# Kernel tuning notes

Measured on AMD Instinct MI355X. Metric: run time of the kernel, lower is better.

Reference implementation:

```python
import jax, jax.numpy as jnp
import numpy as np
import math

DIM, HEADS = 512, 8
D_K = DIM // HEADS

def setup_inputs() -> dict:
    key = jax.random.key(0)
    ks = jax.random.split(key, 6)
    B, LK, LQ = 16, 2048, 256
    s = 1.0 / math.sqrt(DIM)
    return {
        "L": jax.random.normal(ks[0], (B, LK, DIM), jnp.float32),
        "G": jax.random.normal(ks[1], (B, LQ, DIM), jnp.float32),
        "Wq": jax.random.normal(ks[2], (DIM, DIM), jnp.float32) * s,
        "bq": jnp.zeros((DIM,), jnp.float32),
        "Wo": jax.random.normal(ks[3], (DIM, DIM), jnp.float32) * s,
        "bo": jnp.zeros((DIM,), jnp.float32),
    }

def reference(L, G, Wq, bq, Wo, bo):
    B = G.shape[0]
    # Q projection from global tokens; K,V are raw local features split into heads
    q = (G @ Wq + bq).reshape(B, -1, HEADS, D_K)          # [B, Lq, H, d]
    k = L.reshape(B, -1, HEADS, D_K)                      # [B, Lk, H, d]
    v = k
    # double scaling as in source: / sqrt(d_k) * dim**-0.5
    scale = (D_K ** -0.5) * (DIM ** -0.5)
    dots = jnp.einsum("bqhd,bkhd->bhqk", q, k) * scale    # [B, H, Lq, Lk]
    attn = jax.nn.softmax(dots, axis=-1)
    x = jnp.einsum("bhqk,bkhd->bqhd", attn, v)            # [B, Lq, H, d]
    x = x.reshape(B, -1, HEADS * D_K)
    return x @ Wo + bo
```

## Files before the change

### kernel.cpp

```cpp
#include <hip/hip_runtime.h>

#define KSTR 72

typedef __attribute__((ext_vector_type(8))) short short8;
typedef __attribute__((ext_vector_type(4))) float f32x4;

#define EXP2F(x) __builtin_amdgcn_exp2f(x)

__device__ __forceinline__ unsigned short f2bf(float f) {
    union { float f; unsigned u; } v; v.f = f;
    unsigned r = v.u + 0x7fff + ((v.u >> 16) & 1);
    return (unsigned short)(r >> 16);
}
__device__ __forceinline__ unsigned pk2(float a, float b) {
    return (unsigned)f2bf(a) | ((unsigned)f2bf(b) << 16);
}

__global__ __launch_bounds__(256) void conv_prep(const float* __restrict__ Lmat,
                                                 const float* __restrict__ Wq,
                                                 const float* __restrict__ Wo,
                                                 unsigned short* __restrict__ KF,
                                                 unsigned short* __restrict__ VF,
                                                 unsigned short* __restrict__ WqF,
                                                 unsigned short* __restrict__ WoF) {
    const int tid = threadIdx.x;
    if (blockIdx.x >= 4096) {
        const int idx = blockIdx.x - 4096;
        const float* W = (idx >> 7) ? Wo : Wq;
        unsigned short* WF = (idx >> 7) ? WoF : WqF;
        int g = (idx & 127) * 256 + tid;
        int lane = g & 63, ntg = (g >> 6) & 31, kt = g >> 11;
        int c = lane & 15, quad = lane >> 4;
        const float* wp = W + (size_t)(32 * kt + 8 * quad) * 512 + 16 * ntg + c;
        float v[8];
        #pragma unroll
        for (int j = 0; j < 8; j++) v[j] = wp[(size_t)j * 512];
        uint4 u;
        u.x = pk2(v[0], v[1]); u.y = pk2(v[2], v[3]);
        u.z = pk2(v[4], v[5]); u.w = pk2(v[6], v[7]);
        *(uint4*)(WF + (size_t)g * 8) = u;
        return;
    }
    __shared__ unsigned short KFs[4096];
    __shared__ unsigned short VFs[4096];
    const int blk = blockIdx.x;
    const int t = blk & 31, h = (blk >> 5) & 7, b = blk >> 8;
    const int key = tid & 63, wv = tid >> 6;

    const float* src = Lmat + ((size_t)(b * 2048 + 64 * t + key)) * 512 + 64 * h + 16 * wv;
    float4 a0 = *(const float4*)src;
    float4 a1 = *(const float4*)(src + 4);
    float4 a2 = *(const float4*)(src + 8);
    float4 a3 = *(const float4*)(src + 12);
    float vals[16] = {a0.x, a0.y, a0.z, a0.w, a1.x, a1.y, a1.z, a1.w,
                      a2.x, a2.y, a2.z, a2.w, a3.x, a3.y, a3.z, a3.w};
    #pragma unroll
    for (int i = 0; i < 16; i++) {
        int d = 16 * wv + i;
        unsigned short bv = f2bf(vals[i]);
        KFs[((((key >> 4) * 2 + (d >> 5)) * 64) + ((d >> 3) & 3) * 16 + (key & 15)) * 8 + (d & 7)] = bv;
        VFs[((((d >> 4) * 2 + (key >> 5)) * 64) + ((key >> 3) & 3) * 16 + (d & 15)) * 8 + (key & 7)] = bv;
    }
    __syncthreads();
    size_t gbase = (size_t)blk * 4096 + tid * 16;
    *(uint4*)(KF + gbase)     = *(const uint4*)&KFs[tid * 16];
    *(uint4*)(KF + gbase + 8) = *(const uint4*)&KFs[tid * 16 + 8];
    *(uint4*)(VF + gbase)     = *(const uint4*)&VFs[tid * 16];
    *(uint4*)(VF + gbase + 8) = *(const uint4*)&VFs[tid * 16 + 8];
}

template<bool A_BF16, bool OUT_BF16>
__global__ __launch_bounds__(256, 2) void gemm_direct(const void* __restrict__ Ap,
                                                      const unsigned short* __restrict__ WF,
                                                      const float* __restrict__ bias,
                                                      void* __restrict__ Cp,
                                                      float oscale) {
    const int tid = threadIdx.x;
    const int wv = tid >> 6, lane = tid & 63;
    const int c = lane & 15, quad = lane >> 4;
    const int m0 = blockIdx.x * 64, n0 = blockIdx.y * 64;
    const int row = m0 + 16 * wv + c;

    f32x4 acc[4];
    #pragma unroll
    for (int nt = 0; nt < 4; nt++) acc[nt] = (f32x4){0.f, 0.f, 0.f, 0.f};

    #pragma unroll
    for (int kk = 0; kk < 16; kk++) {
        short8 af;
        if (A_BF16) {
            af = *(const short8*)((const unsigned short*)Ap + (size_t)row * 512 + 32 * kk + 8 * quad);
        } else {
            const float* ap = (const float*)Ap + (size_t)row * 512 + 32 * kk + 8 * quad;
            float4 x0 = *(const float4*)ap;
            float4 x1 = *(const float4*)(ap + 4);
            af[0] = (short)f2bf(x0.x); af[1] = (short)f2bf(x0.y);
            af[2] = (short)f2bf(x0.z); af[3] = (short)f2bf(x0.w);
            af[4] = (short)f2bf(x1.x); af[5] = (short)f2bf(x1.y);
            af[6] = (short)f2bf(x1.z); af[7] = (short)f2bf(x1.w);
        }
        #pragma unroll
        for (int nt = 0; nt < 4; nt++) {
            short8 bf = *(const short8*)(WF +
                (((size_t)kk * 32 + (n0 >> 4) + nt) * 64 + lane) * 8);
            acc[nt] = __builtin_amdgcn_mfma_f32_16x16x32_bf16(af, bf, acc[nt], 0, 0, 0);
        }
    }

    #pragma unroll
    for (int nt = 0; nt < 4; nt++) {
        float bv = bias[n0 + 16 * nt + c];
        #pragma unroll
        for (int r = 0; r < 4; r++) {
            float v = (acc[nt][r] + bv) * oscale;
            size_t idx = (size_t)(m0 + 16 * wv + 4 * quad + r) * 512 + n0 + 16 * nt + c;
            if (OUT_BF16) ((unsigned short*)Cp)[idx] = f2bf(v);
            else          ((float*)Cp)[idx] = v;
        }
    }
}

__global__ __launch_bounds__(256, 2) void attn_frag(const float* __restrict__ G,
                                                    const unsigned short* __restrict__ WqF,
                                                    const float* __restrict__ bq,
                                                    const unsigned short* __restrict__ KF,
                                                    const unsigned short* __restrict__ VF,
                                                    unsigned short* __restrict__ X,
                                                    float SCe) {
    __shared__ __align__(16) char shm_raw[4 * 64 * 68 * 4];
    unsigned short (*Pw)[4][16 * KSTR] = (unsigned short (*)[4][16 * KSTR])shm_raw;
    unsigned short (*Qs)[72] = (unsigned short (*)[72])(shm_raw + 36864);
    float (*Mrg)[64][68] = (float (*)[64][68])shm_raw;

    const int raw = blockIdx.x;
    const int h  = raw & 7;
    const int qt = (raw >> 3) & 3;
    const int b  = raw >> 5;
    const int tid = threadIdx.x;
    const int wv = tid >> 6, lane = tid & 63;
    const int c = lane & 15, quad = lane >> 4;
    const int n0 = h * 64;

    {
        f32x4 qacc[4];
        #pragma unroll
        for (int nt = 0; nt < 4; nt++) qacc[nt] = (f32x4){0.f, 0.f, 0.f, 0.f};
        const float* gbase = G + ((size_t)(b * 256 + qt * 64 + 16 * wv + c)) * 512;
        #pragma unroll
        for (int kk = 0; kk < 16; kk++) {
            const float* ap = gbase + 32 * kk + 8 * quad;
            float4 x0 = *(const float4*)ap;
            float4 x1 = *(const float4*)(ap + 4);
            short8 af;
            af[0] = (short)f2bf(x0.x); af[1] = (short)f2bf(x0.y);
            af[2] = (short)f2bf(x0.z); af[3] = (short)f2bf(x0.w);
            af[4] = (short)f2bf(x1.x); af[5] = (short)f2bf(x1.y);
            af[6] = (short)f2bf(x1.z); af[7] = (short)f2bf(x1.w);
            #pragma unroll
            for (int nt = 0; nt < 4; nt++) {
                short8 bf = *(const short8*)(WqF +
                    (((size_t)kk * 32 + (n0 >> 4) + nt) * 64 + lane) * 8);
                qacc[nt] = __builtin_amdgcn_mfma_f32_16x16x32_bf16(af, bf, qacc[nt], 0, 0, 0);
            }
        }
        #pragma unroll
        for (int nt = 0; nt < 4; nt++) {
            float bv = bq[n0 + 16 * nt + c];
            #pragma unroll
            for (int r = 0; r < 4; r++)
                Qs[16 * wv + 4 * quad + r][16 * nt + c] =
                    f2bf((qacc[nt][r] + bv) * SCe);
        }
    }
    __syncthreads();

    short8 qa[4][2];
    #pragma unroll
    for (int g = 0; g < 4; g++) {
        qa[g][0] = *(const short8*)&Qs[16 * g + c][8 * quad];
        qa[g][1] = *(const short8*)&Qs[16 * g + c][32 + 8 * quad];
    }

    short8 ones;
    #pragma unroll
    for (int i = 0; i < 8; i++) ones[i] = (short)0x3F80;

    f32x4 oacc[4][4];
    #pragma unroll
    for (int g = 0; g < 4; g++)
        #pragma unroll
        for (int dt = 0; dt < 4; dt++) oacc[g][dt] = (f32x4){0.f, 0.f, 0.f, 0.f};
    f32x4 lacc[4];
    #pragma unroll
    for (int g = 0; g < 4; g++) lacc[g] = (f32x4){0.f, 0.f, 0.f, 0.f};

    const int swc = (c >> 3) & 1;
    const int swr = (quad >> 1) & 1;

    const unsigned short* kf = KF + ((size_t)((b * 8 + h) * 32)) * 4096 + lane * 8;
    const unsigned short* vf = VF + ((size_t)((b * 8 + h) * 32)) * 4096 + lane * 8;

    for (int i = 0; i < 8; i++) {
        const int T = wv + 4 * i;
        const unsigned short* kt = kf + (size_t)T * 4096;
        const unsigned short* vt = vf + (size_t)T * 4096;
        short8 kbuf[8], vbuf[8];
        #pragma unroll
        for (int f = 0; f < 8; f++) kbuf[f] = *(const short8*)(kt + f * 512);
        #pragma unroll
        for (int f = 0; f < 8; f++) vbuf[f] = *(const short8*)(vt + f * 512);

        #pragma unroll
        for (int g = 0; g < 4; g++) {
            f32x4 sacc[4];
            #pragma unroll
            for (int nt = 0; nt < 4; nt++) sacc[nt] = (f32x4){0.f, 0.f, 0.f, 0.f};
            __builtin_amdgcn_s_setprio(1);
            #pragma unroll
            for (int nt = 0; nt < 4; nt++)
                #pragma unroll
                for (int ks = 0; ks < 2; ks++)
                    sacc[nt] = __builtin_amdgcn_mfma_f32_16x16x32_bf16(
                        qa[g][ks], kbuf[nt * 2 + ks], sacc[nt], 0, 0, 0);
            __builtin_amdgcn_s_setprio(0);
            #pragma unroll
            for (int nt = 0; nt < 4; nt++)
                #pragma unroll
                for (int r = 0; r < 4; r++)
                    Pw[wv][g][(4 * quad + r) * KSTR + ((16 * nt + c) ^ (8 * swr))] =
                        f2bf(EXP2F(sacc[nt][r]));
        }
        #pragma unroll
        for (int g = 0; g < 4; g++) {
            short8 pa0 = *(const short8*)&Pw[wv][g][c * KSTR + 8 * (quad ^ swc)];
            short8 pa1 = *(const short8*)&Pw[wv][g][c * KSTR + 32 + 8 * (quad ^ swc)];
            __builtin_amdgcn_s_setprio(1);
            #pragma unroll
            for (int dt = 0; dt < 4; dt++) {
                oacc[g][dt] = __builtin_amdgcn_mfma_f32_16x16x32_bf16(pa0, vbuf[dt * 2], oacc[g][dt], 0, 0, 0);
                oacc[g][dt] = __builtin_amdgcn_mfma_f32_16x16x32_bf16(pa1, vbuf[dt * 2 + 1], oacc[g][dt], 0, 0, 0);
            }
            lacc[g] = __builtin_amdgcn_mfma_f32_16x16x32_bf16(pa0, ones, lacc[g], 0, 0, 0);
            lacc[g] = __builtin_amdgcn_mfma_f32_16x16x32_bf16(pa1, ones, lacc[g], 0, 0, 0);
            __builtin_amdgcn_s_setprio(0);
        }
    }

    __syncthreads();
    #pragma unroll
    for (int g = 0; g < 4; g++) {
        #pragma unroll
        for (int dt = 0; dt < 4; dt++)
            #pragma unroll
            for (int r = 0; r < 4; r++)
                Mrg[wv][g * 16 + 4 * quad + r][16 * dt + c] = oacc[g][dt][r];
        #pragma unroll
        for (int r = 0; r < 4; r++)
            Mrg[wv][g * 16 + 4 * quad + r][64] = lacc[g][r];
    }
    __syncthreads();
    {
        const int row = 16 * wv + c;
        float sum[16];
        #pragma unroll
        for (int j = 0; j < 16; j++) sum[j] = 0.f;
        float lsum = 0.f;
        #pragma unroll
        for (int ws = 0; ws < 4; ws++) {
            #pragma unroll
            for (int j = 0; j < 16; j++) sum[j] += Mrg[ws][row][16 * quad + j];
            lsum += Mrg[ws][row][64];
        }
        float inv = 1.f / lsum;
        unsigned short us[16];
        #pragma unroll
        for (int j = 0; j < 16; j++) us[j] = f2bf(sum[j] * inv);
        unsigned short* xp =
            X + ((size_t)(b * 256 + qt * 64 + row)) * 512 + h * 64 + 16 * quad;
        *(uint4*)(xp)     = *(uint4*)&us[0];
        *(uint4*)(xp + 8) = *(uint4*)&us[8];
    }
}

extern "C" void kernel_launch(void* const* d_in, const int* in_sizes, int n_in,
                              void* d_out, int out_size, void* d_ws, size_t ws_size,
                              hipStream_t stream) {
    const float* Lmat = (const float*)d_in[0];
    const float* G    = (const float*)d_in[1];
    const float* Wq   = (const float*)d_in[2];
    const float* bq   = (const float*)d_in[3];
    const float* Wo   = (const float*)d_in[4];
    const float* bo   = (const float*)d_in[5];
    float* out = (float*)d_out;

    const float SCe = 0.005524271728019903f * 1.4426950408889634f;

    unsigned short* Qws = (unsigned short*)d_ws;
    unsigned short* Xws = Qws + (size_t)2097152;
    unsigned short* WqF = Xws + (size_t)2097152;
    unsigned short* WoF = WqF + (size_t)262144;
    unsigned short* KF  = WoF + (size_t)262144;
    unsigned short* VF  = KF  + (size_t)16777216;

    conv_prep<<<4352, 256, 0, stream>>>(Lmat, Wq, Wo, KF, VF, WqF, WoF);
    attn_frag<<<512, 256, 0, stream>>>(G, WqF, bq, KF, VF, Xws, SCe);
    gemm_direct<true, false><<<dim3(64, 8), 256, 0, stream>>>(Xws, WoF, bo, out, 1.0f);
}
```

Measured before the change: 164.3 us.

## Stage K/V tiles through LDS with double-buffered async loads, split rows per wave

```diff
diff --git a/kernel.cpp b/kernel.cpp
--- a/kernel.cpp
+++ b/kernel.cpp
@@ -6,6 +6,8 @@
 typedef __attribute__((ext_vector_type(4))) float f32x4;
 
 #define EXP2F(x) __builtin_amdgcn_exp2f(x)
+#define WAITV(n) asm volatile("s_waitcnt vmcnt(" #n ")" ::: "memory")
+#define SCHEDB() __builtin_amdgcn_sched_barrier(0)
 
 __device__ __forceinline__ unsigned short f2bf(float f) {
     union { float f; unsigned u; } v; v.f = f;
@@ -127,10 +129,10 @@
                                                     const unsigned short* __restrict__ VF,
                                                     unsigned short* __restrict__ X,
                                                     float SCe) {
-    __shared__ __align__(16) char shm_raw[4 * 64 * 68 * 4];
-    unsigned short (*Pw)[4][16 * KSTR] = (unsigned short (*)[4][16 * KSTR])shm_raw;
-    unsigned short (*Qs)[72] = (unsigned short (*)[72])(shm_raw + 36864);
-    float (*Mrg)[64][68] = (float (*)[64][68])shm_raw;
+    __shared__ unsigned short Kr[2][4096];
+    __shared__ unsigned short Vr[2][4096];
+    __shared__ unsigned short Pw[4][16 * KSTR];
+    __shared__ unsigned short Qs[64][72];
 
     const int raw = blockIdx.x;
     const int h  = raw & 7;
@@ -174,112 +176,101 @@
     }
     __syncthreads();
 
-    short8 qa[4][2];
-    #pragma unroll
-    for (int g = 0; g < 4; g++) {
-        qa[g][0] = *(const short8*)&Qs[16 * g + c][8 * quad];
-        qa[g][1] = *(const short8*)&Qs[16 * g + c][32 + 8 * quad];
-    }
+    short8 qa[2];
+    qa[0] = *(const short8*)&Qs[16 * wv + c][8 * quad];
+    qa[1] = *(const short8*)&Qs[16 * wv + c][32 + 8 * quad];
 
     short8 ones;
     #pragma unroll
     for (int i = 0; i < 8; i++) ones[i] = (short)0x3F80;
 
-    f32x4 oacc[4][4];
-    #pragma unroll
-    for (int g = 0; g < 4; g++)
-        #pragma unroll
-        for (int dt = 0; dt < 4; dt++) oacc[g][dt] = (f32x4){0.f, 0.f, 0.f, 0.f};
-    f32x4 lacc[4];
-    #pragma unroll
-    for (int g = 0; g < 4; g++) lacc[g] = (f32x4){0.f, 0.f, 0.f, 0.f};
+    f32x4 oacc[4];
+    #pragma unroll
+    for (int dt = 0; dt < 4; dt++) oacc[dt] = (f32x4){0.f, 0.f, 0.f, 0.f};
+    f32x4 lacc = (f32x4){0.f, 0.f, 0.f, 0.f};
 
     const int swc = (c >> 3) & 1;
     const int swr = (quad >> 1) & 1;
 
-    const unsigned short* kf = KF + ((size_t)((b * 8 + h) * 32)) * 4096 + lane * 8;
-    const unsigned short* vf = VF + ((size_t)((b * 8 + h) * 32)) * 4096 + lane * 8;
-
-    for (int i = 0; i < 8; i++) {
-        const int T = wv + 4 * i;
-        const unsigned short* kt = kf + (size_t)T * 4096;
-        const unsigned short* vt = vf + (size_t)T * 4096;
-        short8 kbuf[8], vbuf[8];
-        #pragma unroll
-        for (int f = 0; f < 8; f++) kbuf[f] = *(const short8*)(kt + f * 512);
-        #pragma unroll
-        for (int f = 0; f < 8; f++) vbuf[f] = *(const short8*)(vt + f * 512);
-
-        #pragma unroll
-        for (int g = 0; g < 4; g++) {
-            f32x4 sacc[4];
-            #pragma unroll
-            for (int nt = 0; nt < 4; nt++) sacc[nt] = (f32x4){0.f, 0.f, 0.f, 0.f};
-            __builtin_amdgcn_s_setprio(1);
-            #pragma unroll
-            for (int nt = 0; nt < 4; nt++)
-                #pragma unroll
-                for (int ks = 0; ks < 2; ks++)
-                    sacc[nt] = __builtin_amdgcn_mfma_f32_16x16x32_bf16(
-                        qa[g][ks], kbuf[nt * 2 + ks], sacc[nt], 0, 0, 0);
-            __builtin_amdgcn_s_setprio(0);
-            #pragma unroll
-            for (int nt = 0; nt < 4; nt++)
-                #pragma unroll
-                for (int r = 0; r < 4; r++)
-                    Pw[wv][g][(4 * quad + r) * KSTR + ((16 * nt + c) ^ (8 * swr))] =
-                        f2bf(EXP2F(sacc[nt][r]));
-        }
-        #pragma unroll
-        for (int g = 0; g < 4; g++) {
-            short8 pa0 = *(const short8*)&Pw[wv][g][c * KSTR + 8 * (quad ^ swc)];
-            short8 pa1 = *(const short8*)&Pw[wv][g][c * KSTR + 32 + 8 * (quad ^ swc)];
-            __builtin_amdgcn_s_setprio(1);
-            #pragma unroll
-            for (int dt = 0; dt < 4; dt++) {
-                oacc[g][dt] = __builtin_amdgcn_mfma_f32_16x16x32_bf16(pa0, vbuf[dt * 2], oacc[g][dt], 0, 0, 0);
-                oacc[g][dt] = __builtin_amdgcn_mfma_f32_16x16x32_bf16(pa1, vbuf[dt * 2 + 1], oacc[g][dt], 0, 0, 0);
-            }
-            lacc[g] = __builtin_amdgcn_mfma_f32_16x16x32_bf16(pa0, ones, lacc[g], 0, 0, 0);
-            lacc[g] = __builtin_amdgcn_mfma_f32_16x16x32_bf16(pa1, ones, lacc[g], 0, 0, 0);
-            __builtin_amdgcn_s_setprio(0);
-        }
-    }
-
-    __syncthreads();
-    #pragma unroll
-    for (int g = 0; g < 4; g++) {
+    const unsigned short* kf0 = KF + ((size_t)((b * 8 + h) * 32)) * 4096;
+    const unsigned short* vf0 = VF + ((size_t)((b * 8 + h) * 32)) * 4096;
+
+#define STAGE(bs, tp) do { \
+        const unsigned short* ks_ = kf0 + (size_t)(tp) * 4096 + wv * 1024 + lane * 8; \
+        const unsigned short* vs_ = vf0 + (size_t)(tp) * 4096 + wv * 1024 + lane * 8; \
+        __builtin_amdgcn_global_load_lds((const unsigned int*)ks_, \
+            (unsigned int*)&Kr[bs][wv * 1024 + lane * 8], 16, 0, 0); \
+        __builtin_amdgcn_global_load_lds((const unsigned int*)(ks_ + 512), \
+            (unsigned int*)&Kr[bs][wv * 1024 + 512 + lane * 8], 16, 0, 0); \
+        __builtin_amdgcn_global_load_lds((const unsigned int*)vs_, \
+            (unsigned int*)&Vr[bs][wv * 1024 + lane * 8], 16, 0, 0); \
+        __builtin_amdgcn_global_load_lds((const unsigned int*)(vs_ + 512), \
+            (unsigned int*)&Vr[bs][wv * 1024 + 512 + lane * 8], 16, 0, 0); \
+    } while (0)
+
+    auto compute = [&](const unsigned short* kr, const unsigned short* vr) {
+        short8 kbuf[8];
+        #pragma unroll
+        for (int f = 0; f < 8; f++) kbuf[f] = *(const short8*)(kr + f * 512 + lane * 8);
+        f32x4 sacc[4];
+        #pragma unroll
+        for (int nt = 0; nt < 4; nt++) sacc[nt] = (f32x4){0.f, 0.f, 0.f, 0.f};
+        __builtin_amdgcn_s_setprio(1);
+        #pragma unroll
+        for (int nt = 0; nt < 4; nt++)
+            #pragma unroll
+            for (int ks = 0; ks < 2; ks++)
+                sacc[nt] = __builtin_amdgcn_mfma_f32_16x16x32_bf16(
+                    qa[ks], kbuf[nt * 2 + ks], sacc[nt], 0, 0, 0);
+        __builtin_amdgcn_s_setprio(0);
+        #pragma unroll
+        for (int nt = 0; nt < 4; nt++)
+            #pragma unroll
+            for (int r = 0; r < 4; r++)
+                Pw[wv][(4 * quad + r) * KSTR + ((16 * nt + c) ^ (8 * swr))] =
+                    f2bf(EXP2F(sacc[nt][r]));
+        short8 pa0 = *(const short8*)&Pw[wv][c * KSTR + 8 * (quad ^ swc)];
+        short8 pa1 = *(const short8*)&Pw[wv][c * KSTR + 32 + 8 * (quad ^ swc)];
+        short8 vbuf[8];
+        #pragma unroll
+        for (int f = 0; f < 8; f++) vbuf[f] = *(const short8*)(vr + f * 512 + lane * 8);
+        __builtin_amdgcn_s_setprio(1);
+        #pragma unroll
+        for (int dt = 0; dt < 4; dt++) {
+            oacc[dt] = __builtin_amdgcn_mfma_f32_16x16x32_bf16(pa0, vbuf[dt * 2], oacc[dt], 0, 0, 0);
+            oacc[dt] = __builtin_amdgcn_mfma_f32_16x16x32_bf16(pa1, vbuf[dt * 2 + 1], oacc[dt], 0, 0, 0);
+        }
+        lacc = __builtin_amdgcn_mfma_f32_16x16x32_bf16(pa0, ones, lacc, 0, 0, 0);
+        lacc = __builtin_amdgcn_mfma_f32_16x16x32_bf16(pa1, ones, lacc, 0, 0, 0);
+        __builtin_amdgcn_s_setprio(0);
+    };
+
+    STAGE(0, 0);
+    STAGE(1, 1);
+    for (int i = 0; i < 16; i++) {
+        WAITV(4); SCHEDB();
+        __syncthreads();
+        compute(&Kr[0][0], &Vr[0][0]);
+        __syncthreads();
+        if (i < 15) { STAGE(0, 2 * i + 2); WAITV(4); }
+        else        { WAITV(0); }
+        SCHEDB();
+        __syncthreads();
+        compute(&Kr[1][0], &Vr[1][0]);
+        __syncthreads();
+        if (i < 15) STAGE(1, 2 * i + 3);
+    }
+
+    #pragma unroll
+    for (int r = 0; r < 4; r++) {
+        float inv = 1.f / lacc[r];
+        size_t row = (size_t)(b * 256 + qt * 64 + 16 * wv + 4 * quad + r);
+        unsigned short* xp = X + row * 512 + h * 64;
         #pragma unroll
         for (int dt = 0; dt < 4; dt++)
-            #pragma unroll
-            for (int r = 0; r < 4; r++)
-                Mrg[wv][g * 16 + 4 * quad + r][16 * dt + c] = oacc[g][dt][r];
-        #pragma unroll
-        for (int r = 0; r < 4; r++)
-            Mrg[wv][g * 16 + 4 * quad + r][64] = lacc[g][r];
-    }
-    __syncthreads();
-    {
-        const int row = 16 * wv + c;
-        float sum[16];
-        #pragma unroll
-        for (int j = 0; j < 16; j++) sum[j] = 0.f;
-        float lsum = 0.f;
-        #pragma unroll
-        for (int ws = 0; ws < 4; ws++) {
-            #pragma unroll
-            for (int j = 0; j < 16; j++) sum[j] += Mrg[ws][row][16 * quad + j];
-            lsum += Mrg[ws][row][64];
-        }
-        float inv = 1.f / lsum;
-        unsigned short us[16];
-        #pragma unroll
-        for (int j = 0; j < 16; j++) us[j] = f2bf(sum[j] * inv);
-        unsigned short* xp =
-            X + ((size_t)(b * 256 + qt * 64 + row)) * 512 + h * 64 + 16 * quad;
-        *(uint4*)(xp)     = *(uint4*)&us[0];
-        *(uint4*)(xp + 8) = *(uint4*)&us[8];
-    }
+            xp[16 * dt + c] = f2bf(oacc[dt][r] * inv);
+    }
+#undef STAGE
 }
 
 extern "C" void kernel_launch(void* const* d_in, const int* in_sizes, int n_in,
```

Result: slower. 173.6 us (+5.7%).

## Prefetch K tiles into a double-buffered LDS ring with direct global-to-LDS loads

Applied to the files above, without the earlier changes.

```diff
diff --git a/kernel.cpp b/kernel.cpp
--- a/kernel.cpp
+++ b/kernel.cpp
@@ -6,6 +6,8 @@
 typedef __attribute__((ext_vector_type(4))) float f32x4;
 
 #define EXP2F(x) __builtin_amdgcn_exp2f(x)
+#define WAITV(n) asm volatile("s_waitcnt vmcnt(" #n ")" ::: "memory")
+#define SCHEDB() __builtin_amdgcn_sched_barrier(0)
 
 __device__ __forceinline__ unsigned short f2bf(float f) {
     union { float f; unsigned u; } v; v.f = f;
@@ -127,10 +129,11 @@
                                                     const unsigned short* __restrict__ VF,
                                                     unsigned short* __restrict__ X,
                                                     float SCe) {
-    __shared__ __align__(16) char shm_raw[4 * 64 * 68 * 4];
-    unsigned short (*Pw)[4][16 * KSTR] = (unsigned short (*)[4][16 * KSTR])shm_raw;
-    unsigned short (*Qs)[72] = (unsigned short (*)[72])(shm_raw + 36864);
-    float (*Mrg)[64][68] = (float (*)[64][68])shm_raw;
+    __shared__ __align__(16) char shm[65536 + 9216];
+    unsigned short (*Kring)[2][4096] = (unsigned short (*)[2][4096])shm;
+    unsigned short (*Pw)[16 * KSTR] = (unsigned short (*)[16 * KSTR])(shm + 65536);
+    unsigned short (*Qs)[72] = (unsigned short (*)[72])(shm + 65536);
+    float (*Mrg)[64][68] = (float (*)[64][68])shm;
 
     const int raw = blockIdx.x;
     const int h  = raw & 7;
@@ -140,6 +143,21 @@
     const int wv = tid >> 6, lane = tid & 63;
     const int c = lane & 15, quad = lane >> 4;
     const int n0 = h * 64;
+
+    const unsigned short* kf0 = KF + ((size_t)((b * 8 + h) * 32)) * 4096;
+    const unsigned short* vf0 = VF + ((size_t)((b * 8 + h) * 32)) * 4096;
+
+#define STAGEK(slot, tp) do { \
+        const unsigned short* ks_ = kf0 + (size_t)(tp) * 4096 + lane * 8; \
+        unsigned short* ld_ = &Kring[wv][slot][lane * 8]; \
+        _Pragma("unroll") \
+        for (int ch_ = 0; ch_ < 8; ch_++) \
+            __builtin_amdgcn_global_load_lds((const unsigned int*)(ks_ + ch_ * 512), \
+                (unsigned int*)(ld_ + ch_ * 512), 16, 0, 0); \
+    } while (0)
+
+    STAGEK(0, wv);
+    STAGEK(1, wv + 4);
 
     {
         f32x4 qacc[4];
@@ -180,6 +198,7 @@
         qa[g][0] = *(const short8*)&Qs[16 * g + c][8 * quad];
         qa[g][1] = *(const short8*)&Qs[16 * g + c][32 + 8 * quad];
     }
+    __syncthreads();
 
     short8 ones;
     #pragma unroll
@@ -197,16 +216,17 @@
     const int swc = (c >> 3) & 1;
     const int swr = (quad >> 1) & 1;
 
-    const unsigned short* kf = KF + ((size_t)((b * 8 + h) * 32)) * 4096 + lane * 8;
-    const unsigned short* vf = VF + ((size_t)((b * 8 + h) * 32)) * 4096 + lane * 8;
-
     for (int i = 0; i < 8; i++) {
         const int T = wv + 4 * i;
-        const unsigned short* kt = kf + (size_t)T * 4096;
-        const unsigned short* vt = vf + (size_t)T * 4096;
-        short8 kbuf[8], vbuf[8];
-        #pragma unroll
-        for (int f = 0; f < 8; f++) kbuf[f] = *(const short8*)(kt + f * 512);
+        const int s = i & 1;
+        WAITV(8); SCHEDB();
+
+        short8 kbuf[8];
+        #pragma unroll
+        for (int f = 0; f < 8; f++)
+            kbuf[f] = *(const short8*)&Kring[wv][s][f * 512 + lane * 8];
+        const unsigned short* vt = vf0 + (size_t)T * 4096 + lane * 8;
+        short8 vbuf[8];
         #pragma unroll
         for (int f = 0; f < 8; f++) vbuf[f] = *(const short8*)(vt + f * 512);
 
@@ -227,13 +247,10 @@
             for (int nt = 0; nt < 4; nt++)
                 #pragma unroll
                 for (int r = 0; r < 4; r++)
-                    Pw[wv][g][(4 * quad + r) * KSTR + ((16 * nt + c) ^ (8 * swr))] =
+                    Pw[wv][(4 * quad + r) * KSTR + ((16 * nt + c) ^ (8 * swr))] =
                         f2bf(EXP2F(sacc[nt][r]));
-        }
-        #pragma unroll
-        for (int g = 0; g < 4; g++) {
-            short8 pa0 = *(const short8*)&Pw[wv][g][c * KSTR + 8 * (quad ^ swc)];
-            short8 pa1 = *(const short8*)&Pw[wv][g][c * KSTR + 32 + 8 * (quad ^ swc)];
+            short8 pa0 = *(const short8*)&Pw[wv][c * KSTR + 8 * (quad ^ swc)];
+            short8 pa1 = *(const short8*)&Pw[wv][c * KSTR + 32 + 8 * (quad ^ swc)];
             __builtin_amdgcn_s_setprio(1);
             #pragma unroll
             for (int dt = 0; dt < 4; dt++) {
@@ -244,6 +261,8 @@
             lacc[g] = __builtin_amdgcn_mfma_f32_16x16x32_bf16(pa1, ones, lacc[g], 0, 0, 0);
             __builtin_amdgcn_s_setprio(0);
         }
+
+        if (i < 6) STAGEK(s, T + 8);
     }
 
     __syncthreads();
@@ -280,6 +299,7 @@
         *(uint4*)(xp)     = *(uint4*)&us[0];
         *(uint4*)(xp + 8) = *(uint4*)&us[8];
     }
+#undef STAGEK
 }
 
 extern "C" void kernel_launch(void* const* d_in, const int* in_sizes, int n_in,
```

New measurement: 167.1 us. About the same (+1.7%).

## Use eight waves per attention block and shrink P scratch to one tile per wave

Applied to the files above, without the earlier changes.

```diff
diff --git a/kernel.cpp b/kernel.cpp
--- a/kernel.cpp
+++ b/kernel.cpp
@@ -120,17 +120,17 @@
     }
 }
 
-__global__ __launch_bounds__(256, 2) void attn_frag(const float* __restrict__ G,
+__global__ __launch_bounds__(512, 4) void attn_frag(const float* __restrict__ G,
                                                     const unsigned short* __restrict__ WqF,
                                                     const float* __restrict__ bq,
                                                     const unsigned short* __restrict__ KF,
                                                     const unsigned short* __restrict__ VF,
                                                     unsigned short* __restrict__ X,
                                                     float SCe) {
-    __shared__ __align__(16) char shm_raw[4 * 64 * 68 * 4];
-    unsigned short (*Pw)[4][16 * KSTR] = (unsigned short (*)[4][16 * KSTR])shm_raw;
-    unsigned short (*Qs)[72] = (unsigned short (*)[72])(shm_raw + 36864);
-    float (*Mrg)[64][68] = (float (*)[64][68])shm_raw;
+    __shared__ __align__(16) char shm[4 * 64 * 68 * 4];
+    unsigned short (*Pw)[16 * KSTR] = (unsigned short (*)[16 * KSTR])shm;
+    unsigned short (*Qs)[72] = (unsigned short (*)[72])(shm + 18432);
+    float (*Mrg)[64][68] = (float (*)[64][68])shm;
 
     const int raw = blockIdx.x;
     const int h  = raw & 7;
@@ -141,7 +141,7 @@
     const int c = lane & 15, quad = lane >> 4;
     const int n0 = h * 64;
 
-    {
+    if (wv < 4) {
         f32x4 qacc[4];
         #pragma unroll
         for (int nt = 0; nt < 4; nt++) qacc[nt] = (f32x4){0.f, 0.f, 0.f, 0.f};
@@ -200,8 +200,8 @@
     const unsigned short* kf = KF + ((size_t)((b * 8 + h) * 32)) * 4096 + lane * 8;
     const unsigned short* vf = VF + ((size_t)((b * 8 + h) * 32)) * 4096 + lane * 8;
 
-    for (int i = 0; i < 8; i++) {
-        const int T = wv + 4 * i;
+    for (int i = 0; i < 4; i++) {
+        const int T = wv + 8 * i;
         const unsigned short* kt = kf + (size_t)T * 4096;
         const unsigned short* vt = vf + (size_t)T * 4096;
         short8 kbuf[8], vbuf[8];
@@ -227,13 +227,10 @@
             for (int nt = 0; nt < 4; nt++)
                 #pragma unroll
                 for (int r = 0; r < 4; r++)
-                    Pw[wv][g][(4 * quad + r) * KSTR + ((16 * nt + c) ^ (8 * swr))] =
+                    Pw[wv][(4 * quad + r) * KSTR + ((16 * nt + c) ^ (8 * swr))] =
                         f2bf(EXP2F(sacc[nt][r]));
-        }
-        #pragma unroll
-        for (int g = 0; g < 4; g++) {
-            short8 pa0 = *(const short8*)&Pw[wv][g][c * KSTR + 8 * (quad ^ swc)];
-            short8 pa1 = *(const short8*)&Pw[wv][g][c * KSTR + 32 + 8 * (quad ^ swc)];
+            short8 pa0 = *(const short8*)&Pw[wv][c * KSTR + 8 * (quad ^ swc)];
+            short8 pa1 = *(const short8*)&Pw[wv][c * KSTR + 32 + 8 * (quad ^ swc)];
             __builtin_amdgcn_s_setprio(1);
             #pragma unroll
             for (int dt = 0; dt < 4; dt++) {
@@ -247,19 +244,46 @@
     }
 
     __syncthreads();
-    #pragma unroll
-    for (int g = 0; g < 4; g++) {
-        #pragma unroll
-        for (int dt = 0; dt < 4; dt++)
+    if (wv >= 4) {
+        #pragma unroll
+        for (int g = 0; g < 4; g++) {
+            #pragma unroll
+            for (int dt = 0; dt < 4; dt++)
+                #pragma unroll
+                for (int r = 0; r < 4; r++)
+                    Mrg[wv - 4][g * 16 + 4 * quad + r][16 * dt + c] = oacc[g][dt][r];
             #pragma unroll
             for (int r = 0; r < 4; r++)
-                Mrg[wv][g * 16 + 4 * quad + r][16 * dt + c] = oacc[g][dt][r];
-        #pragma unroll
-        for (int r = 0; r < 4; r++)
-            Mrg[wv][g * 16 + 4 * quad + r][64] = lacc[g][r];
-    }
-    __syncthreads();
-    {
+                Mrg[wv - 4][g * 16 + 4 * quad + r][64] = lacc[g][r];
+        }
+    }
+    __syncthreads();
+    if (wv < 4) {
+        #pragma unroll
+        for (int g = 0; g < 4; g++) {
+            #pragma unroll
+            for (int dt = 0; dt < 4; dt++)
+                #pragma unroll
+                for (int r = 0; r < 4; r++)
+                    oacc[g][dt][r] += Mrg[wv][g * 16 + 4 * quad + r][16 * dt + c];
+            #pragma unroll
+            for (int r = 0; r < 4; r++)
+                lacc[g][r] += Mrg[wv][g * 16 + 4 * quad + r][64];
+        }
+        #pragma unroll
+        for (int g = 0; g < 4; g++) {
+            #pragma unroll
+            for (int dt = 0; dt < 4; dt++)
+                #pragma unroll
+                for (int r = 0; r < 4; r++)
+                    Mrg[wv][g * 16 + 4 * quad + r][16 * dt + c] = oacc[g][dt][r];
+            #pragma unroll
+            for (int r = 0; r < 4; r++)
+                Mrg[wv][g * 16 + 4 * quad + r][64] = lacc[g][r];
+        }
+    }
+    __syncthreads();
+    if (wv < 4) {
         const int row = 16 * wv + c;
         float sum[16];
         #pragma unroll
@@ -303,6 +327,6 @@
     unsigned short* VF  = KF  + (size_t)16777216;
 
     conv_prep<<<4352, 256, 0, stream>>>(Lmat, Wq, Wo, KF, VF, WqF, WoF);
-    attn_frag<<<512, 256, 0, stream>>>(G, WqF, bq, KF, VF, Xws, SCe);
+    attn_frag<<<512, 512, 0, stream>>>(G, WqF, bq, KF, VF, Xws, SCe);
     gemm_direct<true, false><<<dim3(64, 8), 256, 0, stream>>>(Xws, WoF, bo, out, 1.0f);
 }
```

After: 250.2 us. +52.3%, slower.
